# Kernel tuning notes

Measured on AMD Instinct MI355X. Metric: run time of the kernel, lower is better.

## Reference

```python
import jax, jax.numpy as jnp
import numpy as np

WINDOW = 3      # neighbor_cand_window / neighbor_ment_window default
RHO = 1.0
THRED = 0.8     # sim_thred default
EPS = 1e-8      # torch cosine_similarity eps
B, C, D = 2048, 16, 256


def setup_inputs() -> dict:
    key = jax.random.key(0)
    k1, k2 = jax.random.split(key)
    cand_emb = jax.random.normal(k1, (B * C, D), dtype=jnp.float32)
    # num_mentions acts as a 0/1 validity mask per (mention, candidate)
    num_mentions = jax.random.randint(k2, (B, C), 0, 2).astype(jnp.int32)
    return {"cand_emb": cand_emb, "num_mentions": num_mentions}


def _shifted_copies(emb, left_mask, right_mask, window, cand_num):
    # Replicates iterated leftNeighbor / rightNeighbor: shift rows by cand_num
    # and re-apply the mask after every shift (cumulative masking).
    zeros = jnp.zeros((cand_num, emb.shape[1]), emb.dtype)
    lefts, cur = [], emb
    for _ in range(window):
        cur = jnp.concatenate([zeros, cur[:-cand_num]], axis=0) * left_mask
        lefts.append(cur)
    rights, cur = [], emb
    for _ in range(window):
        cur = jnp.concatenate([cur[cand_num:], zeros], axis=0) * right_mask
        rights.append(cur)
    return lefts, rights


def _forward(cand_emb, num_mentions):
    batch_size, cand_num = num_mentions.shape
    dim = cand_emb.shape[1]
    right_mask = num_mentions.astype(cand_emb.dtype)                       # [B, C]
    left_mask = jnp.concatenate(
        [jnp.zeros((1, cand_num), cand_emb.dtype), right_mask[:-1]], axis=0)
    lm = left_mask.reshape(-1, 1)    # [B*C, 1], broadcasts over dim
    rm = right_mask.reshape(-1, 1)

    lefts, rights = _shifted_copies(cand_emb, lm, rm, WINDOW, cand_num)

    # getNeighborMentionEmbeddingsForCandidate: mean over 2*window shifted copies
    neigh_emb = jnp.mean(jnp.stack(lefts + rights, axis=0), axis=0)        # [B*C, D]

    # buildGraph: cosine similarity of each candidate against every candidate
    # of each shifted copy, block-structured (no [N, 2W*C, D] materialization).
    cand3 = cand_emb.reshape(batch_size, cand_num, dim)
    nc = jnp.linalg.norm(cand3, axis=-1)                                   # [B, C]
    parts = []
    for s in lefts + rights:
        s3 = s.reshape(batch_size, cand_num, dim)
        ns = jnp.linalg.norm(s3, axis=-1)                                  # [B, C]
        dot = jnp.einsum('bid,bjd->bij', cand3, s3)
        sim = dot / jnp.maximum(nc[:, :, None] * ns[:, None, :], EPS)
        # clamp(sim, thred, 1) then zero everything <= thred
        sim = jnp.where(sim > THRED, jnp.clip(sim, THRED, 1.0), 0.0)
        parts.append(sim)
    adj = jnp.concatenate(parts, axis=2).reshape(batch_size * cand_num, -1)
    ones_col = jnp.ones((batch_size * cand_num, 1), cand_emb.dtype)
    adj = jnp.concatenate([adj * RHO, ones_col], axis=1)
    adj = adj / jnp.maximum(jnp.sum(jnp.abs(adj), axis=1, keepdims=True), 1e-12)

    # [B*C, D + 2*WINDOW*C + 1]
    return jnp.concatenate([neigh_emb, adj], axis=1)


def reference(cand_emb, num_mentions):
    return _forward(cand_emb, num_mentions)
```

## Files before the change

### kernel.cpp

```cpp
#include <hip/hip_runtime.h>

#define NB 2048
#define NC 16
#define ND 256
#define G  8
#define NT 14
#define TPB 512
#define OUTW 353
#define THRED 0.8f

typedef short bf16x8 __attribute__((ext_vector_type(8)));
typedef unsigned short u16x8 __attribute__((ext_vector_type(8)));
typedef float f32x4 __attribute__((ext_vector_type(4)));

__device__ __forceinline__ unsigned short f2bf(float x) {
    unsigned int u = __float_as_uint(x);
    u += 0x7FFFu + ((u >> 16) & 1u);
    return (unsigned short)(u >> 16);
}
__device__ __forceinline__ float bf2f(unsigned short h) {
    return __uint_as_float(((unsigned int)h) << 16);
}

__global__ __launch_bounds__(TPB) void fused_kernel(const float* __restrict__ e,
                                                    const int* __restrict__ nm,
                                                    float* __restrict__ out) {
    __shared__ __align__(16) unsigned short T[NT * NC * ND];
    __shared__ float norms[NT][NC];
    __shared__ float MskL[G][6][NC];

    const int t  = threadIdx.x;
    const int b0 = blockIdx.x * G;

#pragma unroll
    for (int q = 0; q < (NT * NC * ND / 4) / TPB; ++q) {
        int idx  = q * TPB + t;
        int tile = idx >> 10, rem = idx & 1023;
        int row  = rem >> 6,  c4  = rem & 63;
        int gb   = b0 - 3 + tile;
        ushort4 v = make_ushort4(0, 0, 0, 0);
        if (gb >= 0 && gb < NB) {
            const float4 g = *reinterpret_cast<const float4*>(
                e + (size_t)(gb * NC + row) * ND + c4 * 4);
            v.x = f2bf(g.x); v.y = f2bf(g.y); v.z = f2bf(g.z); v.w = f2bf(g.w);
        }
        int sIdx = tile * 4096 + row * 256 + ((c4 * 4) ^ ((row & 7) << 3));
        *reinterpret_cast<ushort4*>(&T[sIdx]) = v;
    }

    const int w   = t >> 6, l = t & 63;
    const int col = l & 15, hi = l >> 4;
    const int b   = b0 + w;
    float nmv[6];
#pragma unroll
    for (int u = 0; u < 6; ++u) {
        int gb = b + u - 3;
        nmv[u] = (gb >= 0 && gb < NB) ? (float)nm[gb * NC + col] : 0.f;
    }
    float maskv[6];
    maskv[0] = nmv[2];
    maskv[1] = nmv[2] * nmv[1];
    maskv[2] = nmv[2] * nmv[1] * nmv[0];
    maskv[3] = nmv[3];
    maskv[4] = nmv[3] * nmv[4];
    maskv[5] = nmv[3] * nmv[4] * nmv[5];
    if (l < 16) {
#pragma unroll
        for (int p = 0; p < 6; ++p) MskL[w][p][l] = maskv[p];
    }

    __syncthreads();

    if (t < NT * NC) {
        int tile = t >> 4, r = t & 15;
        float ssq = 0.f;
#pragma unroll 8
        for (int k8 = 0; k8 < 32; ++k8) {
            int sIdx = tile * 4096 + r * 256 + ((k8 * 8) ^ ((r & 7) << 3));
            u16x8 vv = *reinterpret_cast<u16x8*>(&T[sIdx]);
#pragma unroll
            for (int ee = 0; ee < 8; ++ee) { float f = bf2f(vv[ee]); ssq = fmaf(f, f, ssq); }
        }
        norms[tile][r] = sqrtf(ssq);
    }
    __syncthreads();

    const int offs[6] = {-1, -2, -3, 1, 2, 3};

    bf16x8 af[8];
#pragma unroll
    for (int c = 0; c < 8; ++c) {
        int sIdx = (w + 3) * 4096 + col * 256 + (((c * 32) + hi * 8) ^ ((col & 7) << 3));
        af[c] = *reinterpret_cast<bf16x8*>(&T[sIdx]);
    }
    f32x4 acc[6];
#pragma unroll
    for (int p = 0; p < 6; ++p) {
        acc[p] = (f32x4){0.f, 0.f, 0.f, 0.f};
        const int tt = w + 3 + offs[p];
#pragma unroll
        for (int c = 0; c < 8; ++c) {
            int sIdx = tt * 4096 + col * 256 + (((c * 32) + hi * 8) ^ ((col & 7) << 3));
            bf16x8 bfr = *reinterpret_cast<bf16x8*>(&T[sIdx]);
            acc[p] = __builtin_amdgcn_mfma_f32_16x16x32_bf16(af[c], bfr, acc[p], 0, 0, 0);
        }
    }

    float na[4];
#pragma unroll
    for (int r4 = 0; r4 < 4; ++r4) na[r4] = norms[w + 3][hi * 4 + r4];

    float sim[6][4];
    float rowsum[4] = {0.f, 0.f, 0.f, 0.f};
#pragma unroll
    for (int p = 0; p < 6; ++p) {
        const int tt = w + 3 + offs[p];
        const float nbv = norms[tt][col];
        const bool mv = (maskv[p] != 0.f);
#pragma unroll
        for (int r4 = 0; r4 < 4; ++r4) {
            float qd = acc[p][r4] / fmaxf(na[r4] * nbv, 1e-8f);
            float s  = (mv && qd > THRED) ? fminf(qd, 1.f) : 0.f;
            sim[p][r4] = s;
            rowsum[r4] += s;
        }
    }
#pragma unroll
    for (int r4 = 0; r4 < 4; ++r4) {
#pragma unroll
        for (int o = 1; o < 16; o <<= 1) rowsum[r4] += __shfl_xor(rowsum[r4], o, 16);
    }

#pragma unroll
    for (int r4 = 0; r4 < 4; ++r4) {
        const float inv = 1.0f / fmaxf(rowsum[r4] + 1.0f, 1e-12f);
        size_t obase = (size_t)(b * NC + hi * 4 + r4) * OUTW;
#pragma unroll
        for (int p = 0; p < 6; ++p)
            out[obase + ND + p * NC + col] = sim[p][r4] * inv;
        if (col == 0) out[obase + ND + 96] = inv;
    }

    const float s6 = 1.0f / 6.0f;
#pragma unroll 4
    for (int r = 0; r < NC; ++r) {
        float a0 = 0.f, a1 = 0.f, a2 = 0.f, a3 = 0.f;
#pragma unroll
        for (int p = 0; p < 6; ++p) {
            const int tt = w + 3 + offs[p];
            const float m = MskL[w][p][r];
            int sIdx = tt * 4096 + r * 256 + ((l * 4) ^ ((r & 7) << 3));
            ushort4 v = *reinterpret_cast<ushort4*>(&T[sIdx]);
            a0 = fmaf(m, bf2f(v.x), a0);
            a1 = fmaf(m, bf2f(v.y), a1);
            a2 = fmaf(m, bf2f(v.z), a2);
            a3 = fmaf(m, bf2f(v.w), a3);
        }
        size_t ob = (size_t)(b * NC + r) * OUTW + l * 4;
        out[ob + 0] = a0 * s6;
        out[ob + 1] = a1 * s6;
        out[ob + 2] = a2 * s6;
        out[ob + 3] = a3 * s6;
    }
}

extern "C" void kernel_launch(void* const* d_in, const int* in_sizes, int n_in,
                              void* d_out, int out_size, void* d_ws, size_t ws_size,
                              hipStream_t stream) {
    const float* e = (const float*)d_in[0];
    const int* nmv = (const int*)d_in[1];
    float* out     = (float*)d_out;
    fused_kernel<<<NB / G, TPB, 0, stream>>>(e, nmv, out);
}
```

Measured before the change: 36.44 us.

## Drop LDS staging; load neighbor tiles directly from global into MFMA registers

Removes the shared-memory tile buffer and both block barriers. Each wave now loads its own and neighbor mention rows straight from global memory into registers and converts them to bf16 for MFMA. Norms and the neighbor mean are accumulated in fp32 from the loaded values. Blocks shrink to 4 waves with a swizzled block index to improve L2 reuse of overlapping neighbor rows. The trade-off is about 7x redundant global reads per row (served by cache), high register pressure from a 64-float accumulator, and strided uncoalesced stores of the neighbor-mean output.

```diff
diff --git a/kernel.cpp b/kernel.cpp
--- a/kernel.cpp
+++ b/kernel.cpp
@@ -3,14 +3,10 @@
 #define NB 2048
 #define NC 16
 #define ND 256
-#define G  8
-#define NT 14
-#define TPB 512
 #define OUTW 353
 #define THRED 0.8f
 
 typedef short bf16x8 __attribute__((ext_vector_type(8)));
-typedef unsigned short u16x8 __attribute__((ext_vector_type(8)));
 typedef float f32x4 __attribute__((ext_vector_type(4)));
 
 __device__ __forceinline__ unsigned short f2bf(float x) {
@@ -18,39 +14,27 @@
     u += 0x7FFFu + ((u >> 16) & 1u);
     return (unsigned short)(u >> 16);
 }
-__device__ __forceinline__ float bf2f(unsigned short h) {
-    return __uint_as_float(((unsigned int)h) << 16);
+
+__device__ __forceinline__ bf16x8 cvt8(const float4& a, const float4& b) {
+    bf16x8 r;
+    r[0] = (short)f2bf(a.x); r[1] = (short)f2bf(a.y);
+    r[2] = (short)f2bf(a.z); r[3] = (short)f2bf(a.w);
+    r[4] = (short)f2bf(b.x); r[5] = (short)f2bf(b.y);
+    r[6] = (short)f2bf(b.z); r[7] = (short)f2bf(b.w);
+    return r;
 }
 
-__global__ __launch_bounds__(TPB) void fused_kernel(const float* __restrict__ e,
-                                                    const int* __restrict__ nm,
-                                                    float* __restrict__ out) {
-    __shared__ __align__(16) unsigned short T[NT * NC * ND];
-    __shared__ float norms[NT][NC];
-    __shared__ float MskL[G][6][NC];
+__global__ __launch_bounds__(256, 2) void fused_kernel(const float* __restrict__ e,
+                                                       const int* __restrict__ nm,
+                                                       float* __restrict__ out) {
+    const int bid = blockIdx.x;
+    const int sb  = (bid & 7) * 64 + (bid >> 3);
+    const int w   = threadIdx.x >> 6;
+    const int l   = threadIdx.x & 63;
+    const int col = l & 15, hi = l >> 4;
+    const int b   = sb * 4 + w;
+    const int koff = hi * 8;
 
-    const int t  = threadIdx.x;
-    const int b0 = blockIdx.x * G;
-
-#pragma unroll
-    for (int q = 0; q < (NT * NC * ND / 4) / TPB; ++q) {
-        int idx  = q * TPB + t;
-        int tile = idx >> 10, rem = idx & 1023;
-        int row  = rem >> 6,  c4  = rem & 63;
-        int gb   = b0 - 3 + tile;
-        ushort4 v = make_ushort4(0, 0, 0, 0);
-        if (gb >= 0 && gb < NB) {
-            const float4 g = *reinterpret_cast<const float4*>(
-                e + (size_t)(gb * NC + row) * ND + c4 * 4);
-            v.x = f2bf(g.x); v.y = f2bf(g.y); v.z = f2bf(g.z); v.w = f2bf(g.w);
-        }
-        int sIdx = tile * 4096 + row * 256 + ((c4 * 4) ^ ((row & 7) << 3));
-        *reinterpret_cast<ushort4*>(&T[sIdx]) = v;
-    }
-
-    const int w   = t >> 6, l = t & 63;
-    const int col = l & 15, hi = l >> 4;
-    const int b   = b0 + w;
     float nmv[6];
 #pragma unroll
     for (int u = 0; u < 6; ++u) {
@@ -60,107 +44,117 @@
     float maskv[6];
     maskv[0] = nmv[2];
     maskv[1] = nmv[2] * nmv[1];
-    maskv[2] = nmv[2] * nmv[1] * nmv[0];
+    maskv[2] = maskv[1] * nmv[0];
     maskv[3] = nmv[3];
     maskv[4] = nmv[3] * nmv[4];
-    maskv[5] = nmv[3] * nmv[4] * nmv[5];
-    if (l < 16) {
+    maskv[5] = maskv[4] * nmv[5];
+
+    const float* rp0 = e + ((size_t)b * NC + col) * ND + koff;
+    float4 s[16];
 #pragma unroll
-        for (int p = 0; p < 6; ++p) MskL[w][p][l] = maskv[p];
+    for (int c = 0; c < 8; ++c) {
+        s[2 * c]     = *reinterpret_cast<const float4*>(rp0 + c * 32);
+        s[2 * c + 1] = *reinterpret_cast<const float4*>(rp0 + c * 32 + 4);
     }
-
-    __syncthreads();
-
-    if (t < NT * NC) {
-        int tile = t >> 4, r = t & 15;
-        float ssq = 0.f;
-#pragma unroll 8
-        for (int k8 = 0; k8 < 32; ++k8) {
-            int sIdx = tile * 4096 + r * 256 + ((k8 * 8) ^ ((r & 7) << 3));
-            u16x8 vv = *reinterpret_cast<u16x8*>(&T[sIdx]);
+    bf16x8 af[8];
+    float ssq = 0.f;
 #pragma unroll
-            for (int ee = 0; ee < 8; ++ee) { float f = bf2f(vv[ee]); ssq = fmaf(f, f, ssq); }
-        }
-        norms[tile][r] = sqrtf(ssq);
+    for (int c = 0; c < 8; ++c) {
+        const float4 a = s[2 * c], bb = s[2 * c + 1];
+        af[c] = cvt8(a, bb);
+        ssq = fmaf(a.x, a.x, ssq);  ssq = fmaf(a.y, a.y, ssq);
+        ssq = fmaf(a.z, a.z, ssq);  ssq = fmaf(a.w, a.w, ssq);
+        ssq = fmaf(bb.x, bb.x, ssq); ssq = fmaf(bb.y, bb.y, ssq);
+        ssq = fmaf(bb.z, bb.z, ssq); ssq = fmaf(bb.w, bb.w, ssq);
     }
-    __syncthreads();
+    ssq += __shfl_xor(ssq, 16, 64);
+    ssq += __shfl_xor(ssq, 32, 64);
+    const float nrm_own = sqrtf(ssq);
 
     const int offs[6] = {-1, -2, -3, 1, 2, 3};
+    f32x4 acc[6];
+    float nbn[6];
+    float nacc[64];
+#pragma unroll
+    for (int q = 0; q < 64; ++q) nacc[q] = 0.f;
 
-    bf16x8 af[8];
-#pragma unroll
-    for (int c = 0; c < 8; ++c) {
-        int sIdx = (w + 3) * 4096 + col * 256 + (((c * 32) + hi * 8) ^ ((col & 7) << 3));
-        af[c] = *reinterpret_cast<bf16x8*>(&T[sIdx]);
-    }
-    f32x4 acc[6];
 #pragma unroll
     for (int p = 0; p < 6; ++p) {
         acc[p] = (f32x4){0.f, 0.f, 0.f, 0.f};
-        const int tt = w + 3 + offs[p];
+        nbn[p] = 0.f;
+        const int gb = b + offs[p];
+        if (gb >= 0 && gb < NB) {
+            const float* rp = e + ((size_t)gb * NC + col) * ND + koff;
 #pragma unroll
-        for (int c = 0; c < 8; ++c) {
-            int sIdx = tt * 4096 + col * 256 + (((c * 32) + hi * 8) ^ ((col & 7) << 3));
-            bf16x8 bfr = *reinterpret_cast<bf16x8*>(&T[sIdx]);
-            acc[p] = __builtin_amdgcn_mfma_f32_16x16x32_bf16(af[c], bfr, acc[p], 0, 0, 0);
+            for (int c = 0; c < 8; ++c) {
+                s[2 * c]     = *reinterpret_cast<const float4*>(rp + c * 32);
+                s[2 * c + 1] = *reinterpret_cast<const float4*>(rp + c * 32 + 4);
+            }
+            float sq = 0.f;
+            const float m = maskv[p];
+#pragma unroll
+            for (int c = 0; c < 8; ++c) {
+                const float4 a = s[2 * c], bb = s[2 * c + 1];
+                bf16x8 bf = cvt8(a, bb);
+                acc[p] = __builtin_amdgcn_mfma_f32_16x16x32_bf16(af[c], bf, acc[p], 0, 0, 0);
+                sq = fmaf(a.x, a.x, sq);  sq = fmaf(a.y, a.y, sq);
+                sq = fmaf(a.z, a.z, sq);  sq = fmaf(a.w, a.w, sq);
+                sq = fmaf(bb.x, bb.x, sq); sq = fmaf(bb.y, bb.y, sq);
+                sq = fmaf(bb.z, bb.z, sq); sq = fmaf(bb.w, bb.w, sq);
+                nacc[c * 8 + 0] = fmaf(m, a.x,  nacc[c * 8 + 0]);
+                nacc[c * 8 + 1] = fmaf(m, a.y,  nacc[c * 8 + 1]);
+                nacc[c * 8 + 2] = fmaf(m, a.z,  nacc[c * 8 + 2]);
+                nacc[c * 8 + 3] = fmaf(m, a.w,  nacc[c * 8 + 3]);
+                nacc[c * 8 + 4] = fmaf(m, bb.x, nacc[c * 8 + 4]);
+                nacc[c * 8 + 5] = fmaf(m, bb.y, nacc[c * 8 + 5]);
+                nacc[c * 8 + 6] = fmaf(m, bb.z, nacc[c * 8 + 6]);
+                nacc[c * 8 + 7] = fmaf(m, bb.w, nacc[c * 8 + 7]);
+            }
+            sq += __shfl_xor(sq, 16, 64);
+            sq += __shfl_xor(sq, 32, 64);
+            nbn[p] = sqrtf(sq);
         }
     }
 
     float na[4];
 #pragma unroll
-    for (int r4 = 0; r4 < 4; ++r4) na[r4] = norms[w + 3][hi * 4 + r4];
+    for (int r = 0; r < 4; ++r) na[r] = __shfl(nrm_own, hi * 4 + r, 16);
 
     float sim[6][4];
     float rowsum[4] = {0.f, 0.f, 0.f, 0.f};
 #pragma unroll
     for (int p = 0; p < 6; ++p) {
-        const int tt = w + 3 + offs[p];
-        const float nbv = norms[tt][col];
         const bool mv = (maskv[p] != 0.f);
 #pragma unroll
-        for (int r4 = 0; r4 < 4; ++r4) {
-            float qd = acc[p][r4] / fmaxf(na[r4] * nbv, 1e-8f);
-            float s  = (mv && qd > THRED) ? fminf(qd, 1.f) : 0.f;
-            sim[p][r4] = s;
-            rowsum[r4] += s;
+        for (int r = 0; r < 4; ++r) {
+            float qd = acc[p][r] / fmaxf(na[r] * nbn[p], 1e-8f);
+            float sv = (mv && qd > THRED) ? fminf(qd, 1.f) : 0.f;
+            sim[p][r] = sv;
+            rowsum[r] += sv;
         }
     }
 #pragma unroll
-    for (int r4 = 0; r4 < 4; ++r4) {
+    for (int r = 0; r < 4; ++r) {
 #pragma unroll
-        for (int o = 1; o < 16; o <<= 1) rowsum[r4] += __shfl_xor(rowsum[r4], o, 16);
+        for (int o = 1; o < 16; o <<= 1) rowsum[r] += __shfl_xor(rowsum[r], o, 16);
     }
 
 #pragma unroll
-    for (int r4 = 0; r4 < 4; ++r4) {
-        const float inv = 1.0f / fmaxf(rowsum[r4] + 1.0f, 1e-12f);
-        size_t obase = (size_t)(b * NC + hi * 4 + r4) * OUTW;
+    for (int r = 0; r < 4; ++r) {
+        const float inv = 1.0f / fmaxf(rowsum[r] + 1.0f, 1e-12f);
+        float* orow = out + (size_t)(b * NC + hi * 4 + r) * OUTW;
 #pragma unroll
-        for (int p = 0; p < 6; ++p)
-            out[obase + ND + p * NC + col] = sim[p][r4] * inv;
-        if (col == 0) out[obase + ND + 96] = inv;
+        for (int p = 0; p < 6; ++p) orow[ND + p * NC + col] = sim[p][r] * inv;
+        if (col == 0) orow[ND + 96] = inv;
     }
 
     const float s6 = 1.0f / 6.0f;
-#pragma unroll 4
-    for (int r = 0; r < NC; ++r) {
-        float a0 = 0.f, a1 = 0.f, a2 = 0.f, a3 = 0.f;
+    float* nrow = out + (size_t)(b * NC + col) * OUTW + koff;
 #pragma unroll
-        for (int p = 0; p < 6; ++p) {
-            const int tt = w + 3 + offs[p];
-            const float m = MskL[w][p][r];
-            int sIdx = tt * 4096 + r * 256 + ((l * 4) ^ ((r & 7) << 3));
-            ushort4 v = *reinterpret_cast<ushort4*>(&T[sIdx]);
-            a0 = fmaf(m, bf2f(v.x), a0);
-            a1 = fmaf(m, bf2f(v.y), a1);
-            a2 = fmaf(m, bf2f(v.z), a2);
-            a3 = fmaf(m, bf2f(v.w), a3);
-        }
-        size_t ob = (size_t)(b * NC + r) * OUTW + l * 4;
-        out[ob + 0] = a0 * s6;
-        out[ob + 1] = a1 * s6;
-        out[ob + 2] = a2 * s6;
-        out[ob + 3] = a3 * s6;
+    for (int c = 0; c < 8; ++c) {
+#pragma unroll
+        for (int ee = 0; ee < 8; ++ee)
+            nrow[c * 32 + ee] = nacc[c * 8 + ee] * s6;
     }
 }
 
@@ -170,5 +164,5 @@
     const float* e = (const float*)d_in[0];
     const int* nmv = (const int*)d_in[1];
     float* out     = (float*)d_out;
-    fused_kernel<<<NB / G, TPB, 0, stream>>>(e, nmv, out);
+    fused_kernel<<<NB / 4, 256, 0, stream>>>(e, nmv, out);
 }
```

Result: slower. 41.45 us (+13.8%).
